# Optimization experiments

Measured on AMD Instinct MI355X. Metric: run time of the kernel, lower is better.

Reference implementation:

```python
import jax, jax.numpy as jnp
import numpy as np

N, E, F = 50000, 800000, 64
GIN_F, H1, H2, OUT = 32, 128, 256, 2


def _lin_init(key, fan_in, fan_out):
    return jax.random.normal(key, (fan_in, fan_out), dtype=jnp.float32) / np.float32(np.sqrt(fan_in))


def setup_inputs() -> dict:
    key = jax.random.key(0)
    ks = jax.random.split(key, 24)
    inp = {
        "x": jax.random.normal(ks[0], (N, F), dtype=jnp.float32),
        "edge_index": jax.random.randint(ks[1], (2, E), 0, N, dtype=jnp.int64),
    }
    # GIN: 3 GINConv layers, each MLP = Linear->ReLU->Linear, then output Linear
    dims = [GIN_F, H1, H1]
    k = 2
    for i, din in enumerate(dims):
        inp[f"g{i}_w1"] = _lin_init(ks[k], din, H1); k += 1
        inp[f"g{i}_b1"] = jnp.zeros((H1,), jnp.float32)
        inp[f"g{i}_w2"] = _lin_init(ks[k], H1, H1); k += 1
        inp[f"g{i}_b2"] = jnp.zeros((H1,), jnp.float32)
    inp["gout_w"] = _lin_init(ks[k], H1, H1); k += 1
    inp["gout_b"] = jnp.zeros((H1,), jnp.float32)
    # SAGE: 2 SAGEConv layers (mean aggregation)
    sdims = [(F + H1, H2), (H2, OUT)]
    for i, (din, dout) in enumerate(sdims):
        inp[f"s{i}_wl"] = _lin_init(ks[k], din, dout); k += 1
        inp[f"s{i}_wr"] = _lin_init(ks[k], din, dout); k += 1
        inp[f"s{i}_b"] = jnp.zeros((dout,), jnp.float32)
    return inp


def _agg_sum(h, src, dst, n):
    # gather messages at src, scatter-add into dst: [N, d]
    return jax.ops.segment_sum(h[src], dst, num_segments=n)


def _forward(x, edge_index, g0_w1, g0_b1, g0_w2, g0_b2, g1_w1, g1_b1, g1_w2, g1_b2,
             g2_w1, g2_b1, g2_w2, g2_b2, gout_w, gout_b,
             s0_wl, s0_wr, s0_b, s1_wl, s1_wr, s1_b):
    src, dst = edge_index[0], edge_index[1]
    n = x.shape[0]
    deg = jax.ops.segment_sum(jnp.ones((src.shape[0],), x.dtype), dst, num_segments=n)
    inv_deg = (1.0 / jnp.maximum(deg, 1.0))[:, None]  # [N,1]

    # GIN branch on selected features (indices 0..31)
    h = x[:, :GIN_F]
    for w1, b1, w2, b2 in ((g0_w1, g0_b1, g0_w2, g0_b2),
                           (g1_w1, g1_b1, g1_w2, g1_b2),
                           (g2_w1, g2_b1, g2_w2, g2_b2)):
        m = h + _agg_sum(h, src, dst, n)        # (1+eps)*x + sum_neigh, eps=0
        h = jax.nn.relu(jax.nn.relu(m @ w1 + b1) @ w2 + b2)
    gin_out = h @ gout_w + gout_b               # [N, H1]

    # concat raw features with GIN embedding
    h = jnp.concatenate([x, gin_out], axis=1)   # [N, F+H1]

    # SAGE branch (mean aggregation)
    mean1 = _agg_sum(h, src, dst, n) * inv_deg
    h = jax.nn.relu(h @ s0_wl + mean1 @ s0_wr + s0_b)
    mean2 = _agg_sum(h, src, dst, n) * inv_deg
    out = h @ s1_wl + mean2 @ s1_wr + s1_b      # [N, OUT]
    return out


def reference(x, edge_index, g0_w1, g0_b1, g0_w2, g0_b2, g1_w1, g1_b1, g1_w2, g1_b2,
              g2_w1, g2_b1, g2_w2, g2_b2, gout_w, gout_b,
              s0_wl, s0_wr, s0_b, s1_wl, s1_wr, s1_b):
    return _forward(x, edge_index, g0_w1, g0_b1, g0_w2, g0_b2, g1_w1, g1_b1, g1_w2, g1_b2,
                    g2_w1, g2_b1, g2_w2, g2_b2, gout_w, gout_b,
                    s0_wl, s0_wr, s0_b, s1_wl, s1_wr, s1_b)
```

## Files before the change

kernel.cpp:

```cpp
#include <hip/hip_runtime.h>


typedef unsigned short ushort_t;
typedef __bf16 bf16x8 __attribute__((ext_vector_type(8)));
typedef float f32x4 __attribute__((ext_vector_type(4)));
typedef unsigned u32x4 __attribute__((ext_vector_type(4)));

__device__ __forceinline__ float b2f(unsigned int u16) {
    union { unsigned int i; float f; } v;
    v.i = u16 << 16;
    return v.f;
}
__device__ __forceinline__ unsigned short f2b(float f) {
    union { float f; unsigned int i; } v;
    v.f = f;
    unsigned int x = v.i;
    unsigned int r = (x + 0x7fffu + ((x >> 16) & 1u)) >> 16;
    return (unsigned short)r;
}

__device__ __forceinline__ void gload_lds16(const void* g, void* l) {
    __builtin_amdgcn_global_load_lds(
        (const __attribute__((address_space(1))) unsigned int*)g,
        (__attribute__((address_space(3))) unsigned int*)l,
        16, 0, 0);
}

__global__ void detect_kernel(const int* __restrict__ ei, int ncheck, int* flag) {
    int t = blockIdx.x * blockDim.x + threadIdx.x;
    if (t < ncheck) {
        if (ei[2 * t + 1] != 0) atomicAnd(flag, 0);
    }
}

__global__ void deg_kernel(const int* __restrict__ ei, int E, const int* __restrict__ flag,
                           int* __restrict__ deg) {
    int e = blockIdx.x * blockDim.x + threadIdx.x;
    if (e >= E) return;
    int d = (*flag) ? ei[2 * ((size_t)E + e)] : ei[(size_t)E + e];
    atomicAdd(&deg[d], 1);
}

__global__ __launch_bounds__(256) void scanA_kernel(const int* __restrict__ deg, int n,
                                                    int* __restrict__ rowptr,
                                                    int* __restrict__ blocksum) {
    __shared__ int sh[256];
    int b = blockIdx.x, tid = threadIdx.x;
    int base = b * 2048 + tid * 8;
    int v[8];
#pragma unroll
    for (int e = 0; e < 8; ++e) {
        int i = base + e;
        v[e] = (i < n) ? deg[i] : 0;
    }
    int t = 0;
#pragma unroll
    for (int e = 0; e < 8; ++e) { int x = v[e]; v[e] = t; t += x; }
    sh[tid] = t;
    __syncthreads();
    for (int off = 1; off < 256; off <<= 1) {
        int val = (tid >= off) ? sh[tid - off] : 0;
        __syncthreads();
        sh[tid] += val;
        __syncthreads();
    }
    int excl = sh[tid] - t;
#pragma unroll
    for (int e = 0; e < 8; ++e) {
        int i = base + e;
        if (i < n) rowptr[i] = excl + v[e];
    }
    if (tid == 255) blocksum[b] = sh[255];
}

__global__ __launch_bounds__(256) void scanB_kernel(const int* __restrict__ blocksum, int nb,
                                                    int* __restrict__ blockoff,
                                                    int* __restrict__ rowptr, int n) {
    __shared__ int sh[256];
    int tid = threadIdx.x;
    int v = (tid < nb) ? blocksum[tid] : 0;
    sh[tid] = v;
    __syncthreads();
    for (int off = 1; off < 256; off <<= 1) {
        int t = (tid >= off) ? sh[tid - off] : 0;
        __syncthreads();
        sh[tid] += t;
        __syncthreads();
    }
    if (tid < nb) blockoff[tid] = sh[tid] - v;
    if (tid == 255) rowptr[n] = sh[255];
}

__global__ void scanC_kernel(const int* __restrict__ deg, int n, const int* __restrict__ blockoff,
                             int* __restrict__ rowptr, float* __restrict__ invdeg,
                             float* __restrict__ mask, int* __restrict__ bucket_cursor) {
    int i = blockIdx.x * blockDim.x + threadIdx.x;
    if (i >= n) return;
    int r = rowptr[i] + blockoff[i >> 11];
    rowptr[i] = r;
    if ((i & 255) == 0) bucket_cursor[i >> 8] = r;
    int d = deg[i];
    invdeg[i] = 1.0f / fmaxf((float)d, 1.0f);
    mask[i] = (d > 0) ? 1.0f : 0.0f;
}

__global__ __launch_bounds__(256) void binA_kernel(
    const int* __restrict__ ei, int E, const int* __restrict__ flag,
    int* __restrict__ bucket_cursor, unsigned* __restrict__ stage) {
    __shared__ unsigned sPair[4096];
    __shared__ int cnt[256], off[256], gst[256];
    int tid = threadIdx.x;
    cnt[tid] = 0;
    __syncthreads();
    int base = blockIdx.x * 4096;
    bool i64 = (*flag) != 0;
    unsigned u[16];
    int bk[16];
#pragma unroll
    for (int k = 0; k < 16; ++k) {
        int e = base + tid + k * 256;
        if (e < E) {
            int s_, d_;
            if (i64) { s_ = ei[2 * (size_t)e]; d_ = ei[2 * ((size_t)E + e)]; }
            else     { s_ = ei[e];             d_ = ei[(size_t)E + e]; }
            bk[k] = d_ >> 8;
            u[k] = (unsigned)s_ | ((unsigned)(d_ & 255) << 16) | ((unsigned)bk[k] << 24);
            atomicAdd(&cnt[bk[k]], 1);
        } else bk[k] = -1;
    }
    __syncthreads();
    int c = cnt[tid];
    off[tid] = c;
    __syncthreads();
    for (int o = 1; o < 256; o <<= 1) {
        int v = (tid >= o) ? off[tid - o] : 0;
        __syncthreads();
        off[tid] += v;
        __syncthreads();
    }
    int incl = off[tid];
    __syncthreads();
    off[tid] = incl - c;
    __syncthreads();
#pragma unroll
    for (int k = 0; k < 16; ++k) {
        if (bk[k] >= 0) {
            int p = atomicAdd(&off[bk[k]], 1);
            sPair[p] = u[k];
        }
    }
    if (c > 0) gst[tid] = atomicAdd(&bucket_cursor[tid], c);
    __syncthreads();
    int total = off[255];
    for (int idx = tid; idx < total; idx += 256) {
        unsigned v = sPair[idx];
        int b = (int)(v >> 24);
        int bstart = off[b] - cnt[b];
        stage[gst[b] + (idx - bstart)] = v;
    }
}

__global__ __launch_bounds__(256) void binB_kernel(
    const unsigned* __restrict__ stage, const int* __restrict__ rowptr,
    int Nn, int* __restrict__ col) {
    __shared__ int curs[256];
    int b = blockIdx.x, tid = threadIdx.x;
    int n0 = b << 8;
    if (n0 + tid < Nn) curs[tid] = rowptr[n0 + tid];
    __syncthreads();
    int s = rowptr[n0];
    int e = rowptr[min(n0 + 256, Nn)];
    for (int i = s + tid; i < e; i += 256) {
        unsigned u = stage[i];
        int p = atomicAdd(&curs[(u >> 16) & 255], 1);
        col[p] = (int)(u & 0xffffu);
    }
}

__global__ void xconv_kernel(const float* __restrict__ x, ushort_t* __restrict__ xb, int total16) {
    int idx = blockIdx.x * blockDim.x + threadIdx.x;
    if (idx >= total16) return;
    float4 v = *(const float4*)&x[(size_t)idx * 4];
    ushort4 u;
    u.x = f2b(v.x); u.y = f2b(v.y); u.z = f2b(v.z); u.w = f2b(v.w);
    *(ushort4*)&xb[(size_t)idx * 4] = u;
}

__global__ void foldw_kernel(const float* __restrict__ gw, const float* __restrict__ gb,
                             const float* __restrict__ s0wl, const float* __restrict__ s0wr,
                             const float* __restrict__ s0bias,
                             float* __restrict__ Fl, float* __restrict__ Fr,
                             float* __restrict__ bias2, float* __restrict__ cvec) {
    int idx = blockIdx.x * blockDim.x + threadIdx.x;
    if (idx >= 128 * 256) return;
    int k = idx >> 8, n = idx & 255;
    const float* wl = s0wl + 64 * 256;
    const float* wr = s0wr + 64 * 256;
    float al = 0.f, ar = 0.f;
    for (int j = 0; j < 128; ++j) {
        float g = gw[k * 128 + j];
        al += g * wl[j * 256 + n];
        ar += g * wr[j * 256 + n];
    }
    Fl[k * 256 + n] = al;
    Fr[k * 256 + n] = ar;
    if (k == 0) {
        float bl = 0.f, br = 0.f;
        for (int j = 0; j < 128; ++j) {
            float g = gb[j];
            bl += g * wl[j * 256 + n];
            br += g * wr[j * 256 + n];
        }
        bias2[n] = s0bias[n] + bl;
        cvec[n] = br;
    }
}

struct WtDesc { const float* src; ushort_t* dst; int lk2; int K; int N; int base; };
struct WtArgs { WtDesc d[10]; int total; };
__global__ void wtconv_kernel(WtArgs a) {
    int idx = blockIdx.x * blockDim.x + threadIdx.x;
    if (idx >= a.total) return;
    int s = 0;
#pragma unroll
    for (int i = 1; i < 10; ++i) if (idx >= a.d[i].base) s = i;
    int local = idx - a.d[s].base;
    int K = a.d[s].K;
    int n = local >> a.d[s].lk2;
    int k = local & (K - 1);
    unsigned off = (unsigned)((n >> 4) * (K >> 5) + (k >> 5)) * 512u
                 + (unsigned)(((n & 15) | (((k >> 3) & 3) << 4)) << 3) + (unsigned)(k & 7);
    a.d[s].dst[off] = f2b(a.d[s].src[(size_t)k * a.d[s].N + n]);
}

template <int VEC>
__device__ __forceinline__ void ldrow(const ushort_t* p, float* t) {
    if constexpr (VEC == 1) {
        t[0] = b2f(p[0]);
    } else if constexpr (VEC == 2) {
        unsigned int v = *(const unsigned int*)p;
        t[0] = b2f(v & 0xffffu); t[1] = b2f(v >> 16);
    } else {
        uint2 v = *(const uint2*)p;
        t[0] = b2f(v.x & 0xffffu); t[1] = b2f(v.x >> 16);
        t[2] = b2f(v.y & 0xffffu); t[3] = b2f(v.y >> 16);
    }
}

template <int VEC, int MODE>
__global__ __launch_bounds__(256) void aggb_kernel(
    const ushort_t* __restrict__ h, int ldh,
    const int* __restrict__ rowptr, const int* __restrict__ col,
    const float* __restrict__ invdeg,
    ushort_t* __restrict__ out, int ldo, int Nn, int lanes) {
    int wid = blockIdx.x * 4 + ((int)threadIdx.x >> 6);
    int lane = (int)threadIdx.x & 63;
    if (wid >= Nn || lane >= lanes) return;

    const ushort_t* hb = h + (size_t)lane * VEC;
    float a[VEC], b2a[VEC];
#pragma unroll
    for (int v = 0; v < VEC; ++v) { a[v] = 0.f; b2a[v] = 0.f; }

    int p0 = __builtin_amdgcn_readfirstlane(rowptr[wid]);
    int p1 = __builtin_amdgcn_readfirstlane(rowptr[wid + 1]);
    int p = p0;
    for (; p + 8 <= p1; p += 8) {
        int j0 = col[p], j1 = col[p + 1], j2 = col[p + 2], j3 = col[p + 3];
        int j4 = col[p + 4], j5 = col[p + 5], j6 = col[p + 6], j7 = col[p + 7];
        float t0[VEC], t1[VEC], t2[VEC], t3[VEC], t4[VEC], t5[VEC], t6[VEC], t7[VEC];
        ldrow<VEC>(hb + (size_t)j0 * ldh, t0);
        ldrow<VEC>(hb + (size_t)j1 * ldh, t1);
        ldrow<VEC>(hb + (size_t)j2 * ldh, t2);
        ldrow<VEC>(hb + (size_t)j3 * ldh, t3);
        ldrow<VEC>(hb + (size_t)j4 * ldh, t4);
        ldrow<VEC>(hb + (size_t)j5 * ldh, t5);
        ldrow<VEC>(hb + (size_t)j6 * ldh, t6);
        ldrow<VEC>(hb + (size_t)j7 * ldh, t7);
#pragma unroll
        for (int v = 0; v < VEC; ++v) {
            a[v]  += (t0[v] + t1[v]) + (t2[v] + t3[v]);
            b2a[v] += (t4[v] + t5[v]) + (t6[v] + t7[v]);
        }
    }
    for (; p + 4 <= p1; p += 4) {
        int j0 = col[p], j1 = col[p + 1], j2 = col[p + 2], j3 = col[p + 3];
        float t0[VEC], t1[VEC], t2[VEC], t3[VEC];
        ldrow<VEC>(hb + (size_t)j0 * ldh, t0);
        ldrow<VEC>(hb + (size_t)j1 * ldh, t1);
        ldrow<VEC>(hb + (size_t)j2 * ldh, t2);
        ldrow<VEC>(hb + (size_t)j3 * ldh, t3);
#pragma unroll
        for (int v = 0; v < VEC; ++v) a[v] += (t0[v] + t1[v]) + (t2[v] + t3[v]);
    }
    for (; p < p1; ++p) {
        float t[VEC];
        ldrow<VEC>(hb + (size_t)col[p] * ldh, t);
#pragma unroll
        for (int v = 0; v < VEC; ++v) a[v] += t[v];
    }
#pragma unroll
    for (int v = 0; v < VEC; ++v) a[v] += b2a[v];

    if constexpr (MODE == 0) {
        float t[VEC];
        ldrow<VEC>(hb + (size_t)wid * ldh, t);
#pragma unroll
        for (int v = 0; v < VEC; ++v) a[v] += t[v];
    } else {
        float s = invdeg[wid];
#pragma unroll
        for (int v = 0; v < VEC; ++v) a[v] *= s;
    }

    ushort_t* op = out + (size_t)wid * ldo + (size_t)lane * VEC;
    if constexpr (VEC == 1) {
        op[0] = f2b(a[0]);
    } else if constexpr (VEC == 2) {
        unsigned int v = (unsigned int)f2b(a[0]) | ((unsigned int)f2b(a[1]) << 16);
        *(unsigned int*)op = v;
    } else {
        uint2 v;
        v.x = (unsigned int)f2b(a[0]) | ((unsigned int)f2b(a[1]) << 16);
        v.y = (unsigned int)f2b(a[2]) | ((unsigned int)f2b(a[3]) << 16);
        *(uint2*)op = v;
    }
}

__global__ __launch_bounds__(256) void aggdual_kernel(
    const ushort_t* __restrict__ xb,
    const int* __restrict__ rowptr, const int* __restrict__ col,
    const float* __restrict__ invdeg,
    ushort_t* __restrict__ out32, ushort_t* __restrict__ out64, int Nn) {
    int wid = blockIdx.x * 4 + ((int)threadIdx.x >> 6);
    int lane = (int)threadIdx.x & 63;
    if (wid >= Nn) return;
    const ushort_t* hb = xb + lane;
    float a = 0.f, b2a = 0.f;
    int p0 = __builtin_amdgcn_readfirstlane(rowptr[wid]);
    int p1 = __builtin_amdgcn_readfirstlane(rowptr[wid + 1]);
    int p = p0;
    for (; p + 8 <= p1; p += 8) {
        float v0 = b2f(hb[(size_t)col[p] * 64]);
        float v1 = b2f(hb[(size_t)col[p + 1] * 64]);
        float v2 = b2f(hb[(size_t)col[p + 2] * 64]);
        float v3 = b2f(hb[(size_t)col[p + 3] * 64]);
        float v4 = b2f(hb[(size_t)col[p + 4] * 64]);
        float v5 = b2f(hb[(size_t)col[p + 5] * 64]);
        float v6 = b2f(hb[(size_t)col[p + 6] * 64]);
        float v7 = b2f(hb[(size_t)col[p + 7] * 64]);
        a += (v0 + v1) + (v2 + v3);
        b2a += (v4 + v5) + (v6 + v7);
    }
    for (; p + 4 <= p1; p += 4) {
        float v0 = b2f(hb[(size_t)col[p] * 64]);
        float v1 = b2f(hb[(size_t)col[p + 1] * 64]);
        float v2 = b2f(hb[(size_t)col[p + 2] * 64]);
        float v3 = b2f(hb[(size_t)col[p + 3] * 64]);
        a += (v0 + v1) + (v2 + v3);
    }
    for (; p < p1; ++p) a += b2f(hb[(size_t)col[p] * 64]);
    a += b2a;
    out64[(size_t)wid * 64 + lane] = f2b(a * invdeg[wid]);
    if (lane < 32) {
        float self = b2f(hb[(size_t)wid * 64]);
        out32[(size_t)wid * 32 + lane] = f2b(a + self);
    }
}

struct GPass { const ushort_t* A; const ushort_t* Wp; int lda; int K; };
struct FArgs {
    GPass p[4]; int np;
    const ushort_t* W2p;
    const float* b1; const float* b2;
    int relu1, relu2;
    int chain;
    const float* rowmask; const float* cvec;
};

__global__ __launch_bounds__(512) void fgemm_kernel(
    FArgs fa, int M, ushort_t* __restrict__ out, int ldc) {
    __shared__ __align__(16) ushort_t Tlds[8192];
    __shared__ __align__(16) ushort_t Wlds[16384];

    int rowbase = blockIdx.x * 64;
    int colbase = blockIdx.y * 128;
    int tid = threadIdx.x;
    int lane = tid & 63, w = tid >> 6;
    int wr3 = w & 3, wc2 = w >> 2;
    int lr = lane & 15, rq = (lane >> 4) * 4;

    f32x4 acc[4];
#pragma unroll
    for (int j = 0; j < 4; ++j) acc[j] = (f32x4){0.f, 0.f, 0.f, 0.f};

    u32x4 w2a = (u32x4){0u,0u,0u,0u}, w2b = w2a, w2c = w2a, w2d = w2a;

    for (int q = 0; q < fa.np; ++q) {
        const ushort_t* A = fa.p[q].A;
        const ushort_t* Wp = fa.p[q].Wp;
        int lda = fa.p[q].lda, K = fa.p[q].K;
        int nch = K >> 5;

        {
            const ushort_t* wsrc = &Wp[((size_t)(colbase >> 4) * nch) * 512];
            for (int j = 0; j < nch; ++j) {
                int i = w * 64 + j * 512;
                gload_lds16(wsrc + (size_t)(i + lane) * 8, &Wlds[i * 8]);
            }
        }
        for (int s = w; s < nch * 4; s += 8) {
            int c = s >> 2, rgrp = s & 3;
            int gr = rowbase + rgrp * 16 + lr;
            int gcol = c * 32 + (lane >> 4) * 8;
            if (gr < M)
                gload_lds16(&A[(size_t)gr * lda + gcol], &Tlds[c * 2048 + rgrp * 512]);
        }
        if (q == 0 && fa.chain >= 2) {
            const u32x4* w2src = (const u32x4*)fa.W2p;
            w2a = w2src[tid];
            w2b = w2src[tid + 512];
            w2c = w2src[tid + 1024];
            w2d = w2src[tid + 1536];
        }
        __syncthreads();
        int cgl0 = wc2 * 4;
        for (int c = 0; c < nch; ++c) {
            bf16x8 af = *(const bf16x8*)&Tlds[c * 2048 + wr3 * 512 + lane * 8];
            bf16x8 bfr[4];
#pragma unroll
            for (int j = 0; j < 4; ++j)
                bfr[j] = *(const bf16x8*)&Wlds[(((cgl0 + j) * nch) + c) * 512 + lane * 8];
#pragma unroll
            for (int j = 0; j < 4; ++j)
                acc[j] = __builtin_amdgcn_mfma_f32_16x16x32_bf16(af, bfr[j], acc[j], 0, 0, 0);
        }
        __syncthreads();
    }

    if (fa.chain >= 2) {
        ((u32x4*)Wlds)[tid] = w2a;
        ((u32x4*)Wlds)[tid + 512] = w2b;
        ((u32x4*)Wlds)[tid + 1024] = w2c;
        ((u32x4*)Wlds)[tid + 1536] = w2d;
#pragma unroll
        for (int j = 0; j < 4; ++j) {
            int colj = wc2 * 64 + j * 16 + lr;
            float bv = fa.b1[colj];
            int kk = colj & 31;
            int cof = (colj >> 5) * 2048 + ((((kk >> 3) << 4)) << 3) + (kk & 7);
#pragma unroll
            for (int t = 0; t < 4; ++t) {
                int row = wr3 * 16 + rq + t;
                float v = acc[j][t] + bv;
                if (fa.relu1) v = fmaxf(v, 0.f);
                Tlds[cof + wr3 * 512 + ((row & 15) << 3)] = f2b(v);
            }
            acc[j] = (f32x4){0.f, 0.f, 0.f, 0.f};
        }
        __syncthreads();
        int cgl0 = wc2 * 4;
        for (int c = 0; c < 4; ++c) {
            bf16x8 af = *(const bf16x8*)&Tlds[c * 2048 + wr3 * 512 + lane * 8];
            bf16x8 bfr[4];
#pragma unroll
            for (int j = 0; j < 4; ++j)
                bfr[j] = *(const bf16x8*)&Wlds[((cgl0 + j) * 4 + c) * 512 + lane * 8];
#pragma unroll
            for (int j = 0; j < 4; ++j)
                acc[j] = __builtin_amdgcn_mfma_f32_16x16x32_bf16(af, bfr[j], acc[j], 0, 0, 0);
        }
        __syncthreads();
    }

    const float* bf_ = (fa.chain == 1) ? fa.b1 : fa.b2;
    int reluf = (fa.chain == 1) ? fa.relu1 : fa.relu2;
    float rm[4];
#pragma unroll
    for (int t = 0; t < 4; ++t) {
        int gr = rowbase + wr3 * 16 + rq + t;
        rm[t] = (fa.cvec && gr < M) ? fa.rowmask[gr] : 0.f;
    }
#pragma unroll
    for (int j = 0; j < 4; ++j) {
        int colj = wc2 * 64 + j * 16 + lr;
        float bv = bf_[colbase + colj];
        float cv = fa.cvec ? fa.cvec[colbase + colj] : 0.f;
#pragma unroll
        for (int t = 0; t < 4; ++t) {
            int row = wr3 * 16 + rq + t;
            float v = acc[j][t] + bv + rm[t] * cv;
            if (reluf) v = fmaxf(v, 0.f);
            Tlds[row * 128 + colj] = f2b(v);
        }
    }
    __syncthreads();
    for (int u = tid; u < 1024; u += 512) {
        int row = u >> 4, seg = u & 15;
        int gr = rowbase + row;
        if (gr < M)
            *(u32x4*)&out[(size_t)gr * ldc + colbase + seg * 8] =
                *(const u32x4*)&Tlds[row * 128 + seg * 8];
    }
}

__global__ void zproj_kernel(const ushort_t* __restrict__ s0,
                             const float* __restrict__ wl, const float* __restrict__ wr,
                             float2* __restrict__ zl, float2* __restrict__ z, int M) {
    int wave = threadIdx.x >> 6;
    int lane = threadIdx.x & 63;
    int i = blockIdx.x * 4 + wave;
    if (i >= M) return;
    float l0 = 0.f, l1 = 0.f, r0 = 0.f, r1 = 0.f;
    for (int k = lane; k < 256; k += 64) {
        float hv = b2f(s0[(size_t)i * 256 + k]);
        float2 wlv = *(const float2*)&wl[2 * k];
        float2 wrv = *(const float2*)&wr[2 * k];
        l0 += hv * wlv.x; l1 += hv * wlv.y;
        r0 += hv * wrv.x; r1 += hv * wrv.y;
    }
#pragma unroll
    for (int off = 32; off > 0; off >>= 1) {
        l0 += __shfl_down(l0, off);
        l1 += __shfl_down(l1, off);
        r0 += __shfl_down(r0, off);
        r1 += __shfl_down(r1, off);
    }
    if (lane == 0) {
        zl[i] = make_float2(l0, l1);
        z[i] = make_float2(r0, r1);
    }
}

__global__ void aggz_kernel(const float2* __restrict__ z, const float2* __restrict__ zl,
                            const int* __restrict__ rowptr, const int* __restrict__ col,
                            const float* __restrict__ invdeg, const float* __restrict__ b,
                            float* __restrict__ out, int Nn) {
    int i = blockIdx.x * blockDim.x + threadIdx.x;
    if (i >= Nn) return;
    float s0 = 0.f, s1 = 0.f;
    int p = rowptr[i], p1 = rowptr[i + 1];
    for (; p + 4 <= p1; p += 4) {
        float2 a = z[col[p]], c = z[col[p + 1]], d = z[col[p + 2]], e = z[col[p + 3]];
        s0 += (a.x + c.x) + (d.x + e.x);
        s1 += (a.y + c.y) + (d.y + e.y);
    }
    for (; p < p1; ++p) {
        float2 a = z[col[p]];
        s0 += a.x; s1 += a.y;
    }
    float inv = invdeg[i];
    float2 l = zl[i];
    out[(size_t)i * 2 + 0] = l.x + inv * s0 + b[0];
    out[(size_t)i * 2 + 1] = l.y + inv * s1 + b[1];
}

extern "C" void kernel_launch(void* const* d_in, const int* in_sizes, int n_in,
                              void* d_out, int out_size, void* d_ws, size_t ws_size,
                              hipStream_t stream) {
    const float* x      = (const float*)d_in[0];
    const int*   ei     = (const int*)d_in[1];
    const float* g_w1[3] = {(const float*)d_in[2], (const float*)d_in[6],  (const float*)d_in[10]};
    const float* g_b1[3] = {(const float*)d_in[3], (const float*)d_in[7],  (const float*)d_in[11]};
    const float* g_w2[3] = {(const float*)d_in[4], (const float*)d_in[8],  (const float*)d_in[12]};
    const float* g_b2[3] = {(const float*)d_in[5], (const float*)d_in[9],  (const float*)d_in[13]};
    const float* gout_w = (const float*)d_in[14];
    const float* gout_b = (const float*)d_in[15];
    const float* s0_wl  = (const float*)d_in[16];
    const float* s0_wr  = (const float*)d_in[17];
    const float* s0_b   = (const float*)d_in[18];
    const float* s1_wl  = (const float*)d_in[19];
    const float* s1_wr  = (const float*)d_in[20];
    const float* s1_b   = (const float*)d_in[21];
    float* out = (float*)d_out;

    const int N = in_sizes[0] / 64;
    const int E = in_sizes[1] / 2;

    char* ws = (char*)d_ws;
    size_t o = 0;
    auto take = [&](size_t bytes) -> char* {
        char* p = ws + o;
        o = (o + bytes + 255) & ~(size_t)255;
        return p;
    };
    ushort_t* xb     = (ushort_t*)take((size_t)N * 64 * 2);
    ushort_t* bA     = (ushort_t*)take((size_t)N * 128 * 2);
    ushort_t* bB     = (ushort_t*)take((size_t)N * 128 * 2);
    ushort_t* bC     = (ushort_t*)take((size_t)N * 128 * 2);
    ushort_t* aggxb  = (ushort_t*)take((size_t)N * 64 * 2);
    ushort_t* agggb  = (ushort_t*)take((size_t)N * 128 * 2);
    ushort_t* s0b    = (ushort_t*)take((size_t)N * 256 * 2);
    float2*   zlb    = (float2*)take((size_t)N * 2 * 4);
    float2*   zb     = (float2*)take((size_t)N * 2 * 4);
    float* Flbuf = (float*)take(128 * 256 * 4);
    float* Frbuf = (float*)take(128 * 256 * 4);
    float* bias2 = (float*)take(256 * 4);
    float* cvecb = (float*)take(256 * 4);
    ushort_t* w1t0 = (ushort_t*)take(128 * 32 * 2);
    ushort_t* w2t0 = (ushort_t*)take(128 * 128 * 2);
    ushort_t* w1t1 = (ushort_t*)take(128 * 128 * 2);
    ushort_t* w2t1 = (ushort_t*)take(128 * 128 * 2);
    ushort_t* w1t2 = (ushort_t*)take(128 * 128 * 2);
    ushort_t* w2t2 = (ushort_t*)take(128 * 128 * 2);
    ushort_t* wltop = (ushort_t*)take(256 * 64 * 2);
    ushort_t* wglp  = (ushort_t*)take(256 * 128 * 2);
    ushort_t* wrtop = (ushort_t*)take(256 * 64 * 2);
    ushort_t* wgrp  = (ushort_t*)take(256 * 128 * 2);
    unsigned* stage  = (unsigned*)take((size_t)E * 4);
    int*   colI   = (int*)take((size_t)E * 4);
    int*   rowptr = (int*)take((size_t)(N + 1) * 4);
    int*   deg    = (int*)take((size_t)N * 4);
    float* invdeg = (float*)take((size_t)N * 4);
    float* maskb  = (float*)take((size_t)N * 4);
    int*   blocksum = (int*)take(256 * 4);
    int*   blockoff = (int*)take(256 * 4);
    int*   bucket_cursor = (int*)take(512 * 4);
    int*   flag   = (int*)take(4);

    hipMemsetAsync(deg, 0, (size_t)N * 4, stream);
    hipMemsetAsync(flag, 1, 4, stream);

    const int TB = 256;
    const int nb = (N + 2047) / 2048;
    const int NBKT = (N + 255) >> 8;

    detect_kernel<<<4, TB, 0, stream>>>(ei, 1024, flag);
    deg_kernel<<<(E + TB - 1) / TB, TB, 0, stream>>>(ei, E, flag, deg);
    scanA_kernel<<<nb, 256, 0, stream>>>(deg, N, rowptr, blocksum);
    scanB_kernel<<<1, 256, 0, stream>>>(blocksum, nb, blockoff, rowptr, N);
    scanC_kernel<<<(N + TB - 1) / TB, TB, 0, stream>>>(deg, N, blockoff, rowptr, invdeg, maskb, bucket_cursor);
    binA_kernel<<<(E + 4095) / 4096, 256, 0, stream>>>(ei, E, flag, bucket_cursor, stage);
    binB_kernel<<<NBKT, 256, 0, stream>>>(stage, rowptr, N, colI);

    foldw_kernel<<<128, 256, 0, stream>>>(gout_w, gout_b, s0_wl, s0_wr, s0_b,
                                          Flbuf, Frbuf, bias2, cvecb);
    WtArgs wa;
    const float* wsrc[10] = {g_w1[0], g_w2[0], g_w1[1], g_w2[1], g_w1[2], g_w2[2],
                             s0_wl, Flbuf, s0_wr, Frbuf};
    ushort_t* wdst[10]    = {w1t0, w2t0, w1t1, w2t1, w1t2, w2t2,
                             wltop, wglp, wrtop, wgrp};
    int wk[10]  = {32, 128, 128, 128, 128, 128, 64, 128, 64, 128};
    int wl2[10] = {5, 7, 7, 7, 7, 7, 6, 7, 6, 7};
    int wn[10]  = {128, 128, 128, 128, 128, 128, 256, 256, 256, 256};
    int base = 0;
    for (int i = 0; i < 10; ++i) {
        wa.d[i].src = wsrc[i]; wa.d[i].dst = wdst[i];
        wa.d[i].lk2 = wl2[i]; wa.d[i].K = wk[i]; wa.d[i].N = wn[i]; wa.d[i].base = base;
        base += wk[i] * wn[i];
    }
    wa.total = base;
    wtconv_kernel<<<(base + TB - 1) / TB, TB, 0, stream>>>(wa);

    xconv_kernel<<<((N * 16) + TB - 1) / TB, TB, 0, stream>>>(x, xb, N * 16);

    const int AGG_GRID = (N + 3) / 4;
    const int GX = (N + 63) / 64;

    aggdual_kernel<<<AGG_GRID, 256, 0, stream>>>(xb, rowptr, colI, invdeg, bB, aggxb, N);

    {
        FArgs fa = {};
        fa.p[0] = {bB, w1t0, 32, 32};
        fa.np = 1;
        fa.W2p = w2t0;
        fa.b1 = g_b1[0]; fa.b2 = g_b2[0];
        fa.relu1 = 1; fa.relu2 = 1;
        fa.chain = 2;
        fgemm_kernel<<<dim3(GX, 1), 512, 0, stream>>>(fa, N, bA, 128);
    }

    aggb_kernel<2, 0><<<AGG_GRID, 256, 0, stream>>>(bA, 128, rowptr, colI, invdeg, bB, 128, N, 64);
    {
        FArgs fa = {};
        fa.p[0] = {bB, w1t1, 128, 128};
        fa.np = 1;
        fa.W2p = w2t1;
        fa.b1 = g_b1[1]; fa.b2 = g_b2[1];
        fa.relu1 = 1; fa.relu2 = 1;
        fa.chain = 2;
        fgemm_kernel<<<dim3(GX, 1), 512, 0, stream>>>(fa, N, bC, 128);
    }

    aggb_kernel<2, 0><<<AGG_GRID, 256, 0, stream>>>(bC, 128, rowptr, colI, invdeg, bB, 128, N, 64);
    {
        FArgs fa = {};
        fa.p[0] = {bB, w1t2, 128, 128};
        fa.np = 1;
        fa.W2p = w2t2;
        fa.b1 = g_b1[2]; fa.b2 = g_b2[2];
        fa.relu1 = 1; fa.relu2 = 1;
        fa.chain = 2;
        fgemm_kernel<<<dim3(GX, 1), 512, 0, stream>>>(fa, N, bA, 128);
    }

    aggb_kernel<2, 1><<<AGG_GRID, 256, 0, stream>>>(bA, 128, rowptr, colI, invdeg, agggb, 128, N, 64);

    {
        FArgs fa = {};
        fa.p[0] = {xb, wltop, 64, 64};
        fa.p[1] = {bA, wglp, 128, 128};
        fa.p[2] = {aggxb, wrtop, 64, 64};
        fa.p[3] = {agggb, wgrp, 128, 128};
        fa.np = 4;
        fa.b1 = bias2;
        fa.relu1 = 1;
        fa.chain = 1;
        fa.rowmask = maskb; fa.cvec = cvecb;
        fgemm_kernel<<<dim3(GX, 2), 512, 0, stream>>>(fa, N, s0b, 256);
    }

    zproj_kernel<<<(N + 3) / 4, 256, 0, stream>>>(s0b, s1_wl, s1_wr, zlb, zb, N);
    aggz_kernel<<<(N + TB - 1) / TB, TB, 0, stream>>>(zb, zlb, rowptr, colI, invdeg, s1_b, out, N);
}
```

Measured before the change: 323.1 us.

## Fuse SAGE layer-2 projection into first SAGE GEMM epilogue via atomics

Result: no change. 327.1 us (+1.2%).

```diff
diff --git a/kernel.cpp b/kernel.cpp
--- a/kernel.cpp
+++ b/kernel.cpp
@@ -376,6 +376,8 @@
     int relu1, relu2;
     int chain;
     const float* rowmask; const float* cvec;
+    const float* pwl; const float* pwr;
+    float* pzl; float* pz;
 };
 
 __global__ __launch_bounds__(512) void fgemm_kernel(
@@ -481,6 +483,56 @@
         int gr = rowbase + wr3 * 16 + rq + t;
         rm[t] = (fa.cvec && gr < M) ? fa.rowmask[gr] : 0.f;
     }
+
+    if (fa.pzl) {
+        float part[4][4];
+#pragma unroll
+        for (int t = 0; t < 4; ++t)
+#pragma unroll
+            for (int k = 0; k < 4; ++k) part[t][k] = 0.f;
+#pragma unroll
+        for (int j = 0; j < 4; ++j) {
+            int c = colbase + wc2 * 64 + j * 16 + lr;
+            float bv = bf_[c];
+            float cv = fa.cvec ? fa.cvec[c] : 0.f;
+            float wl0 = fa.pwl[2 * c], wl1 = fa.pwl[2 * c + 1];
+            float wr0 = fa.pwr[2 * c], wr1 = fa.pwr[2 * c + 1];
+#pragma unroll
+            for (int t = 0; t < 4; ++t) {
+                float v = acc[j][t] + bv + rm[t] * cv;
+                if (reluf) v = fmaxf(v, 0.f);
+                part[t][0] += v * wl0;
+                part[t][1] += v * wl1;
+                part[t][2] += v * wr0;
+                part[t][3] += v * wr1;
+            }
+        }
+#pragma unroll
+        for (int t = 0; t < 4; ++t)
+#pragma unroll
+            for (int k = 0; k < 4; ++k) {
+                float s = part[t][k];
+                s += __shfl_xor(s, 1);
+                s += __shfl_xor(s, 2);
+                s += __shfl_xor(s, 4);
+                s += __shfl_xor(s, 8);
+                part[t][k] = s;
+            }
+        if (lr == 0) {
+#pragma unroll
+            for (int t = 0; t < 4; ++t) {
+                int gr = rowbase + wr3 * 16 + rq + t;
+                if (gr < M) {
+                    atomicAdd(&fa.pzl[2 * gr], part[t][0]);
+                    atomicAdd(&fa.pzl[2 * gr + 1], part[t][1]);
+                    atomicAdd(&fa.pz[2 * gr], part[t][2]);
+                    atomicAdd(&fa.pz[2 * gr + 1], part[t][3]);
+                }
+            }
+        }
+        return;
+    }
+
 #pragma unroll
     for (int j = 0; j < 4; ++j) {
         int colj = wc2 * 64 + j * 16 + lr;
@@ -501,34 +553,6 @@
         if (gr < M)
             *(u32x4*)&out[(size_t)gr * ldc + colbase + seg * 8] =
                 *(const u32x4*)&Tlds[row * 128 + seg * 8];
-    }
-}
-
-__global__ void zproj_kernel(const ushort_t* __restrict__ s0,
-                             const float* __restrict__ wl, const float* __restrict__ wr,
-                             float2* __restrict__ zl, float2* __restrict__ z, int M) {
-    int wave = threadIdx.x >> 6;
-    int lane = threadIdx.x & 63;
-    int i = blockIdx.x * 4 + wave;
-    if (i >= M) return;
-    float l0 = 0.f, l1 = 0.f, r0 = 0.f, r1 = 0.f;
-    for (int k = lane; k < 256; k += 64) {
-        float hv = b2f(s0[(size_t)i * 256 + k]);
-        float2 wlv = *(const float2*)&wl[2 * k];
-        float2 wrv = *(const float2*)&wr[2 * k];
-        l0 += hv * wlv.x; l1 += hv * wlv.y;
-        r0 += hv * wrv.x; r1 += hv * wrv.y;
-    }
-#pragma unroll
-    for (int off = 32; off > 0; off >>= 1) {
-        l0 += __shfl_down(l0, off);
-        l1 += __shfl_down(l1, off);
-        r0 += __shfl_down(r0, off);
-        r1 += __shfl_down(r1, off);
-    }
-    if (lane == 0) {
-        zl[i] = make_float2(l0, l1);
-        z[i] = make_float2(r0, r1);
     }
 }
 
@@ -590,7 +614,6 @@
     ushort_t* bC     = (ushort_t*)take((size_t)N * 128 * 2);
     ushort_t* aggxb  = (ushort_t*)take((size_t)N * 64 * 2);
     ushort_t* agggb  = (ushort_t*)take((size_t)N * 128 * 2);
-    ushort_t* s0b    = (ushort_t*)take((size_t)N * 256 * 2);
     float2*   zlb    = (float2*)take((size_t)N * 2 * 4);
     float2*   zb     = (float2*)take((size_t)N * 2 * 4);
     float* Flbuf = (float*)take(128 * 256 * 4);
@@ -620,6 +643,8 @@
 
     hipMemsetAsync(deg, 0, (size_t)N * 4, stream);
     hipMemsetAsync(flag, 1, 4, stream);
+    hipMemsetAsync(zlb, 0, (size_t)N * 2 * 4, stream);
+    hipMemsetAsync(zb, 0, (size_t)N * 2 * 4, stream);
 
     const int TB = 256;
     const int nb = (N + 2047) / 2048;
@@ -707,9 +732,10 @@
         fa.relu1 = 1;
         fa.chain = 1;
         fa.rowmask = maskb; fa.cvec = cvecb;
-        fgemm_kernel<<<dim3(GX, 2), 512, 0, stream>>>(fa, N, s0b, 256);
-    }
-
-    zproj_kernel<<<(N + 3) / 4, 256, 0, stream>>>(s0b, s1_wl, s1_wr, zlb, zb, N);
+        fa.pwl = s1_wl; fa.pwr = s1_wr;
+        fa.pzl = (float*)zlb; fa.pz = (float*)zb;
+        fgemm_kernel<<<dim3(GX, 2), 512, 0, stream>>>(fa, N, nullptr, 0);
+    }
+
     aggz_kernel<<<(N + TB - 1) / TB, TB, 0, stream>>>(zb, zlb, rowptr, colI, invdeg, s1_b, out, N);
 }
```
